# Kernel optimization log

Hardware: AMD Instinct MI355X
Metric: run time of the kernel (lower is better)

Reference implementation:

```python
import jax, jax.numpy as jnp
import numpy as np

HIDDEN = 32  # hard-coded in EdgeModel's Sequential

def setup_inputs() -> dict:
    key = jax.random.key(0)
    ks = jax.random.split(key, 9)
    E, FN, FE, OUT = 200000, 512, 256, 128
    IN = FN + FN + FE  # 1280
    src = jax.random.normal(ks[0], (E, FN), dtype=jnp.float32)
    dest = jax.random.normal(ks[1], (E, FN), dtype=jnp.float32)
    edge_attr = jax.random.normal(ks[2], (E, FE), dtype=jnp.float32)
    u = jax.random.normal(ks[3], (64, 128), dtype=jnp.float32)
    batch = jax.random.randint(ks[4], (E,), 0, 64, dtype=jnp.int64)
    # Linear params, PyTorch default init scale ~ 1/sqrt(fan_in)
    s1 = 1.0 / np.sqrt(IN)
    s2 = 1.0 / np.sqrt(HIDDEN)
    W1 = jax.random.uniform(ks[5], (IN, HIDDEN), jnp.float32, -s1, s1)
    b1 = jax.random.uniform(ks[6], (HIDDEN,), jnp.float32, -s1, s1)
    W2 = jax.random.uniform(ks[7], (HIDDEN, OUT), jnp.float32, -s2, s2)
    b2 = jax.random.uniform(ks[8], (OUT,), jnp.float32, -s2, s2)
    return {"src": src, "dest": dest, "edge_attr": edge_attr, "u": u,
            "batch": batch, "W1": W1, "b1": b1, "W2": W2, "b2": b2}

def reference(src, dest, edge_attr, u, batch, W1, b1, W2, b2):
    # concat along feature dim, then Linear -> ELU -> Linear (u, batch unused)
    x = jnp.concatenate([src, dest, edge_attr], axis=1)  # [E, 2*FN+FE]
    h = jax.nn.elu(x @ W1 + b1)                           # [E, 32]
    return h @ W2 + b2                                    # [E, OUT]
```

## Files before the change

### kernel.cpp

```cpp
#include <hip/hip_runtime.h>
#include <hip/hip_bf16.h>

typedef __bf16 bf16x8 __attribute__((ext_vector_type(8)));
typedef unsigned short u16x8 __attribute__((ext_vector_type(8)));
typedef float f32x4 __attribute__((ext_vector_type(4)));

__global__ __launch_bounds__(256) void prep_w_kernel(
    const float* __restrict__ W1, const float* __restrict__ W2,
    unsigned short* __restrict__ wsB1, unsigned short* __restrict__ wsB2) {
  int tid = blockIdx.x * 256 + threadIdx.x;
  if (tid < 40960) {
    int j = tid & 7, l = (tid >> 3) & 63, nt = (tid >> 9) & 1, kt = tid >> 10;
    int k = kt * 32 + ((l >> 4) << 3) + j;
    int n = nt * 16 + (l & 15);
    __bf16 v = (__bf16)W1[k * 32 + n];
    wsB1[tid] = __builtin_bit_cast(unsigned short, v);
  } else if (tid < 45056) {
    int t = tid - 40960;
    int j = t & 7, l = (t >> 3) & 63, nt = t >> 9;
    int k = ((l >> 4) << 3) + j;
    int n = nt * 16 + (l & 15);
    __bf16 v = (__bf16)W2[k * 128 + n];
    wsB2[t] = __builtin_bit_cast(unsigned short, v);
  }
}

template <bool USE_WS>
__global__ __launch_bounds__(256) void edge_mlp_kernel(
    const float* __restrict__ src, const float* __restrict__ dst,
    const float* __restrict__ ea, const float* __restrict__ W1,
    const float* __restrict__ b1, const float* __restrict__ W2,
    const float* __restrict__ b2, const unsigned short* __restrict__ wsB1,
    const unsigned short* __restrict__ wsB2, float* __restrict__ out, int nE) {
  __shared__ alignas(16) unsigned short hbuf_s[4][16 * 40];
  const int lane = threadIdx.x & 63;
  const int wave = threadIdx.x >> 6;
  const int l15 = lane & 15;
  const int lh = lane >> 4;
  const long strip = (long)blockIdx.x * 4 + wave;
  const long e0 = strip * 16;
  if (e0 >= nE) return;
  long row = e0 + l15;
  if (row >= nE) row = nE - 1;

  f32x4 acc0 = {0.f, 0.f, 0.f, 0.f};
  f32x4 acc1 = {0.f, 0.f, 0.f, 0.f};

  auto do_tile = [&](const float* p, int kt) {
    f32x4 lo = *(const f32x4*)p;
    f32x4 hi = *(const f32x4*)(p + 4);
    bf16x8 a;
    a[0] = (__bf16)lo[0]; a[1] = (__bf16)lo[1];
    a[2] = (__bf16)lo[2]; a[3] = (__bf16)lo[3];
    a[4] = (__bf16)hi[0]; a[5] = (__bf16)hi[1];
    a[6] = (__bf16)hi[2]; a[7] = (__bf16)hi[3];
    bf16x8 bf0, bf1;
    if (USE_WS) {
      const unsigned short* wp = wsB1 + kt * 1024 + lane * 8;
      bf0 = __builtin_bit_cast(bf16x8, *(const u16x8*)wp);
      bf1 = __builtin_bit_cast(bf16x8, *(const u16x8*)(wp + 512));
    } else {
#pragma unroll
      for (int j = 0; j < 8; ++j) {
        int k = kt * 32 + lh * 8 + j;
        bf0[j] = (__bf16)W1[k * 32 + l15];
        bf1[j] = (__bf16)W1[k * 32 + 16 + l15];
      }
    }
    acc0 = __builtin_amdgcn_mfma_f32_16x16x32_bf16(a, bf0, acc0, 0, 0, 0);
    acc1 = __builtin_amdgcn_mfma_f32_16x16x32_bf16(a, bf1, acc1, 0, 0, 0);
  };

  {
    const float* base = src + row * 512 + lh * 8;
#pragma unroll 4
    for (int kt = 0; kt < 16; ++kt) do_tile(base + kt * 32, kt);
  }
  {
    const float* base = dst + row * 512 + lh * 8;
#pragma unroll 4
    for (int kt = 0; kt < 16; ++kt) do_tile(base + kt * 32, 16 + kt);
  }
  {
    const float* base = ea + row * 256 + lh * 8;
#pragma unroll 4
    for (int kt = 0; kt < 8; ++kt) do_tile(base + kt * 32, 32 + kt);
  }

  const float bias0 = b1[l15];
  const float bias1 = b1[16 + l15];
  unsigned short* hl = hbuf_s[wave];
#pragma unroll
  for (int r = 0; r < 4; ++r) {
    int hrow = lh * 4 + r;
    float h0 = acc0[r] + bias0;
    float h1 = acc1[r] + bias1;
    h0 = h0 > 0.f ? h0 : (__expf(h0) - 1.f);
    h1 = h1 > 0.f ? h1 : (__expf(h1) - 1.f);
    __bf16 v0 = (__bf16)h0, v1 = (__bf16)h1;
    hl[hrow * 40 + l15] = __builtin_bit_cast(unsigned short, v0);
    hl[hrow * 40 + 16 + l15] = __builtin_bit_cast(unsigned short, v1);
  }
  asm volatile("s_waitcnt lgkmcnt(0)" ::: "memory");
  bf16x8 ha =
      __builtin_bit_cast(bf16x8, *(const u16x8*)(hl + l15 * 40 + lh * 8));

  f32x4 o[8];
#pragma unroll
  for (int nt = 0; nt < 8; ++nt) {
    bf16x8 bw;
    if (USE_WS) {
      bw = __builtin_bit_cast(bf16x8, *(const u16x8*)(wsB2 + nt * 512 + lane * 8));
    } else {
#pragma unroll
      for (int j = 0; j < 8; ++j)
        bw[j] = (__bf16)W2[(lh * 8 + j) * 128 + nt * 16 + l15];
    }
    f32x4 z = {0.f, 0.f, 0.f, 0.f};
    o[nt] = __builtin_amdgcn_mfma_f32_16x16x32_bf16(ha, bw, z, 0, 0, 0);
  }

#pragma unroll
  for (int nt = 0; nt < 8; ++nt) {
    float bb = b2[nt * 16 + l15];
#pragma unroll
    for (int r = 0; r < 4; ++r) {
      long e = e0 + lh * 4 + r;
      if (e < nE) out[e * 128 + nt * 16 + l15] = o[nt][r] + bb;
    }
  }
}

extern "C" void kernel_launch(void* const* d_in, const int* in_sizes, int n_in,
                              void* d_out, int out_size, void* d_ws,
                              size_t ws_size, hipStream_t stream) {
  const float* src = (const float*)d_in[0];
  const float* dst = (const float*)d_in[1];
  const float* ea = (const float*)d_in[2];
  const float* W1 = (const float*)d_in[5];
  const float* b1 = (const float*)d_in[6];
  const float* W2 = (const float*)d_in[7];
  const float* b2 = (const float*)d_in[8];
  float* out = (float*)d_out;

  const int nE = in_sizes[0] / 512;
  const long strips = (nE + 15) / 16;
  const int nblocks = (int)((strips + 3) / 4);

  unsigned short* wsB1 = (unsigned short*)d_ws;
  unsigned short* wsB2 = wsB1 + 40960;
  const bool use_ws = ws_size >= 45056 * sizeof(unsigned short);

  if (use_ws) {
    prep_w_kernel<<<176, 256, 0, stream>>>(W1, W2, wsB1, wsB2);
    edge_mlp_kernel<true><<<nblocks, 256, 0, stream>>>(
        src, dst, ea, W1, b1, W2, b2, wsB1, wsB2, out, nE);
  } else {
    edge_mlp_kernel<false><<<nblocks, 256, 0, stream>>>(
        src, dst, ea, W1, b1, W2, b2, nullptr, nullptr, out, nE);
  }
}
```

Measured before the change: 259.5 us.

## Software-pipeline activation and weight loads with register prefetch ring in first GEMM

Replaces the three per-input K loops (unroll 4) with one fully unrolled 40-step loop. It uses a register ring buffer that prefetches activation tiles 6 steps ahead and weight tiles 3 steps ahead. The goal is to keep more global loads in flight and hide memory latency behind the MFMAs in this bandwidth-bound kernel. The cost is higher VGPR pressure, which could lower occupancy.

```diff
diff --git a/kernel.cpp b/kernel.cpp
--- a/kernel.cpp
+++ b/kernel.cpp
@@ -43,48 +43,73 @@
   long row = e0 + l15;
   if (row >= nE) row = nE - 1;
 
+  const float* psrc = src + row * 512 + lh * 8;
+  const float* pdst = dst + row * 512 + lh * 8;
+  const float* pea = ea + row * 256 + lh * 8;
+  const unsigned short* pw1 = wsB1 + lane * 8;
+
   f32x4 acc0 = {0.f, 0.f, 0.f, 0.f};
   f32x4 acc1 = {0.f, 0.f, 0.f, 0.f};
 
-  auto do_tile = [&](const float* p, int kt) {
-    f32x4 lo = *(const f32x4*)p;
-    f32x4 hi = *(const f32x4*)(p + 4);
+  auto xptr = [&](int t) -> const float* {
+    return (t < 16) ? (psrc + t * 32)
+         : (t < 32) ? (pdst + (t - 16) * 32)
+                    : (pea + (t - 32) * 32);
+  };
+
+  constexpr int DX = 6;
+  constexpr int DW = 3;
+  f32x4 px[DX][2];
+  u16x8 pw[DW][2];
+
+#pragma unroll
+  for (int t = 0; t < DX; ++t) {
+    const float* p = xptr(t);
+    px[t][0] = *(const f32x4*)p;
+    px[t][1] = *(const f32x4*)(p + 4);
+  }
+  if constexpr (USE_WS) {
+#pragma unroll
+    for (int t = 0; t < DW; ++t) {
+      pw[t][0] = *(const u16x8*)(pw1 + t * 1024);
+      pw[t][1] = *(const u16x8*)(pw1 + t * 1024 + 512);
+    }
+  }
+
+#pragma unroll
+  for (int t = 0; t < 40; ++t) {
+    f32x4 lo = px[t % DX][0];
+    f32x4 hi = px[t % DX][1];
+    bf16x8 bf0, bf1;
+    if constexpr (USE_WS) {
+      bf0 = __builtin_bit_cast(bf16x8, pw[t % DW][0]);
+      bf1 = __builtin_bit_cast(bf16x8, pw[t % DW][1]);
+    } else {
+#pragma unroll
+      for (int j = 0; j < 8; ++j) {
+        int k = t * 32 + lh * 8 + j;
+        bf0[j] = (__bf16)W1[k * 32 + l15];
+        bf1[j] = (__bf16)W1[k * 32 + 16 + l15];
+      }
+    }
+    if (t + DX < 40) {
+      const float* p = xptr(t + DX);
+      px[t % DX][0] = *(const f32x4*)p;
+      px[t % DX][1] = *(const f32x4*)(p + 4);
+    }
+    if constexpr (USE_WS) {
+      if (t + DW < 40) {
+        pw[t % DW][0] = *(const u16x8*)(pw1 + (t + DW) * 1024);
+        pw[t % DW][1] = *(const u16x8*)(pw1 + (t + DW) * 1024 + 512);
+      }
+    }
     bf16x8 a;
     a[0] = (__bf16)lo[0]; a[1] = (__bf16)lo[1];
     a[2] = (__bf16)lo[2]; a[3] = (__bf16)lo[3];
     a[4] = (__bf16)hi[0]; a[5] = (__bf16)hi[1];
     a[6] = (__bf16)hi[2]; a[7] = (__bf16)hi[3];
-    bf16x8 bf0, bf1;
-    if (USE_WS) {
-      const unsigned short* wp = wsB1 + kt * 1024 + lane * 8;
-      bf0 = __builtin_bit_cast(bf16x8, *(const u16x8*)wp);
-      bf1 = __builtin_bit_cast(bf16x8, *(const u16x8*)(wp + 512));
-    } else {
-#pragma unroll
-      for (int j = 0; j < 8; ++j) {
-        int k = kt * 32 + lh * 8 + j;
-        bf0[j] = (__bf16)W1[k * 32 + l15];
-        bf1[j] = (__bf16)W1[k * 32 + 16 + l15];
-      }
-    }
     acc0 = __builtin_amdgcn_mfma_f32_16x16x32_bf16(a, bf0, acc0, 0, 0, 0);
     acc1 = __builtin_amdgcn_mfma_f32_16x16x32_bf16(a, bf1, acc1, 0, 0, 0);
-  };
-
-  {
-    const float* base = src + row * 512 + lh * 8;
-#pragma unroll 4
-    for (int kt = 0; kt < 16; ++kt) do_tile(base + kt * 32, kt);
-  }
-  {
-    const float* base = dst + row * 512 + lh * 8;
-#pragma unroll 4
-    for (int kt = 0; kt < 16; ++kt) do_tile(base + kt * 32, 16 + kt);
-  }
-  {
-    const float* base = ea + row * 256 + lh * 8;
-#pragma unroll 4
-    for (int kt = 0; kt < 8; ++kt) do_tile(base + kt * 32, 32 + kt);
   }
 
   const float bias0 = b1[l15];
```

Result: no change. 259.6 us (+0.0%).

## Software-pipeline input and weight loads with inline-asm buffer loads and explicit vmcnt waits

Applied to the files above, without the earlier changes.

Replaces the compiler-scheduled loop over the 40 K-tiles with a hand-unrolled software pipeline. It uses inline-asm buffer_load_dwordx4 with buffer resource descriptors, six activation slots and four weight slots in flight, and explicit s_waitcnt vmcnt gating each MFMA pair. The aim is to keep many global loads outstanding per wave so the memory-bound streaming of the 1280-wide rows hides latency. It also sets a minimum-occupancy launch bound and adds scheduling barriers. In exchange it raises register pressure, and the 32-bit buffer descriptor sizes could overflow for larger edge counts.

```diff
diff --git a/kernel.cpp b/kernel.cpp
--- a/kernel.cpp
+++ b/kernel.cpp
@@ -4,6 +4,7 @@
 typedef __bf16 bf16x8 __attribute__((ext_vector_type(8)));
 typedef unsigned short u16x8 __attribute__((ext_vector_type(8)));
 typedef float f32x4 __attribute__((ext_vector_type(4)));
+typedef unsigned int u32x4 __attribute__((ext_vector_type(4)));
 
 __global__ __launch_bounds__(256) void prep_w_kernel(
     const float* __restrict__ W1, const float* __restrict__ W2,
@@ -25,8 +26,46 @@
   }
 }
 
+__device__ __forceinline__ u32x4 make_srd(const void* p, unsigned bytes) {
+  u32x4 r;
+  r[0] = (unsigned)(unsigned long long)p;
+  r[1] = (unsigned)(((unsigned long long)p) >> 32);
+  r[2] = bytes;
+  r[3] = 0x00020000u;
+  return r;
+}
+
+#define XLD(SLOT, VOFF, OFF0, OFF1)                                        \
+  asm volatile("buffer_load_dwordx4 %0, %2, %3, 0 offen offset:" #OFF0     \
+               "\n\tbuffer_load_dwordx4 %1, %2, %3, 0 offen offset:" #OFF1 \
+               : "=&v"(px[SLOT][0]), "=&v"(px[SLOT][1])                    \
+               : "v"(VOFF), "s"(srdX))
+#define WLD(SLOT, SOFF)                                                    \
+  asm volatile("buffer_load_dwordx4 %0, %2, %3, %4 offen offset:0"         \
+               "\n\tbuffer_load_dwordx4 %1, %2, %3, %4 offen offset:1024"  \
+               : "=&v"(pw[SLOT][0]), "=&v"(pw[SLOT][1])                    \
+               : "v"(voffw), "s"(srdw), "s"((unsigned)(SOFF)))
+#define VMW(N)                                                \
+  do {                                                        \
+    asm volatile("s_waitcnt vmcnt(" #N ")" ::: "memory");     \
+    __builtin_amdgcn_sched_barrier(0);                        \
+  } while (0)
+#define CONS(SX, SW)                                                          \
+  do {                                                                        \
+    f32x4 lo = px[SX][0], hi = px[SX][1];                                     \
+    bf16x8 a;                                                                 \
+    a[0] = (__bf16)lo[0]; a[1] = (__bf16)lo[1];                               \
+    a[2] = (__bf16)lo[2]; a[3] = (__bf16)lo[3];                               \
+    a[4] = (__bf16)hi[0]; a[5] = (__bf16)hi[1];                               \
+    a[6] = (__bf16)hi[2]; a[7] = (__bf16)hi[3];                               \
+    acc0 = __builtin_amdgcn_mfma_f32_16x16x32_bf16(                           \
+        a, __builtin_bit_cast(bf16x8, pw[SW][0]), acc0, 0, 0, 0);             \
+    acc1 = __builtin_amdgcn_mfma_f32_16x16x32_bf16(                           \
+        a, __builtin_bit_cast(bf16x8, pw[SW][1]), acc1, 0, 0, 0);             \
+  } while (0)
+
 template <bool USE_WS>
-__global__ __launch_bounds__(256) void edge_mlp_kernel(
+__global__ __launch_bounds__(256, 4) void edge_mlp_kernel(
     const float* __restrict__ src, const float* __restrict__ dst,
     const float* __restrict__ ea, const float* __restrict__ W1,
     const float* __restrict__ b1, const float* __restrict__ W2,
@@ -46,45 +85,95 @@
   f32x4 acc0 = {0.f, 0.f, 0.f, 0.f};
   f32x4 acc1 = {0.f, 0.f, 0.f, 0.f};
 
-  auto do_tile = [&](const float* p, int kt) {
-    f32x4 lo = *(const f32x4*)p;
-    f32x4 hi = *(const f32x4*)(p + 4);
-    bf16x8 a;
-    a[0] = (__bf16)lo[0]; a[1] = (__bf16)lo[1];
-    a[2] = (__bf16)lo[2]; a[3] = (__bf16)lo[3];
-    a[4] = (__bf16)hi[0]; a[5] = (__bf16)hi[1];
-    a[6] = (__bf16)hi[2]; a[7] = (__bf16)hi[3];
-    bf16x8 bf0, bf1;
-    if (USE_WS) {
-      const unsigned short* wp = wsB1 + kt * 1024 + lane * 8;
-      bf0 = __builtin_bit_cast(bf16x8, *(const u16x8*)wp);
-      bf1 = __builtin_bit_cast(bf16x8, *(const u16x8*)(wp + 512));
-    } else {
+  if constexpr (USE_WS) {
+    const u32x4 srdS = make_srd(src, (unsigned)nE * 2048u);
+    const u32x4 srdD = make_srd(dst, (unsigned)nE * 2048u);
+    const u32x4 srdE = make_srd(ea, (unsigned)nE * 1024u);
+    const u32x4 srdw = make_srd(wsB1, 81920u);
+    const unsigned voffx = (unsigned)row * 2048u + (unsigned)lh * 32u;
+    const unsigned voffe = (unsigned)row * 1024u + (unsigned)lh * 32u;
+    const unsigned voffw = (unsigned)lane * 16u;
+
+    f32x4 px[6][2];
+    u16x8 pw[4][2];
+
+    {
+      const u32x4 srdX = srdS;
+      XLD(0, voffx, 0, 16);       WLD(0, 0);
+      XLD(1, voffx, 128, 144);    WLD(1, 2048);
+      XLD(2, voffx, 256, 272);    WLD(2, 4096);
+      XLD(3, voffx, 384, 400);    WLD(3, 6144);
+      XLD(4, voffx, 512, 528);
+      XLD(5, voffx, 640, 656);
+
+      VMW(16); CONS(0, 0); XLD(0, voffx, 768, 784);    WLD(0, 8192);
+      VMW(16); CONS(1, 1); XLD(1, voffx, 896, 912);    WLD(1, 10240);
+      VMW(16); CONS(2, 2); XLD(2, voffx, 1024, 1040);  WLD(2, 12288);
+      VMW(16); CONS(3, 3); XLD(3, voffx, 1152, 1168);  WLD(3, 14336);
+      VMW(12); CONS(4, 0); XLD(4, voffx, 1280, 1296);  WLD(0, 16384);
+      VMW(12); CONS(5, 1); XLD(5, voffx, 1408, 1424);  WLD(1, 18432);
+      VMW(12); CONS(0, 2); XLD(0, voffx, 1536, 1552);  WLD(2, 20480);
+      VMW(12); CONS(1, 3); XLD(1, voffx, 1664, 1680);  WLD(3, 22528);
+      VMW(12); CONS(2, 0); XLD(2, voffx, 1792, 1808);  WLD(0, 24576);
+      VMW(12); CONS(3, 1); XLD(3, voffx, 1920, 1936);  WLD(1, 26624);
+    }
+    {
+      const u32x4 srdX = srdD;
+      VMW(12); CONS(4, 2); XLD(4, voffx, 0, 16);       WLD(2, 28672);
+      VMW(12); CONS(5, 3); XLD(5, voffx, 128, 144);    WLD(3, 30720);
+      VMW(12); CONS(0, 0); XLD(0, voffx, 256, 272);    WLD(0, 32768);
+      VMW(12); CONS(1, 1); XLD(1, voffx, 384, 400);    WLD(1, 34816);
+      VMW(12); CONS(2, 2); XLD(2, voffx, 512, 528);    WLD(2, 36864);
+      VMW(12); CONS(3, 3); XLD(3, voffx, 640, 656);    WLD(3, 38912);
+      VMW(12); CONS(4, 0); XLD(4, voffx, 768, 784);    WLD(0, 40960);
+      VMW(12); CONS(5, 1); XLD(5, voffx, 896, 912);    WLD(1, 43008);
+      VMW(12); CONS(0, 2); XLD(0, voffx, 1024, 1040);  WLD(2, 45056);
+      VMW(12); CONS(1, 3); XLD(1, voffx, 1152, 1168);  WLD(3, 47104);
+      VMW(12); CONS(2, 0); XLD(2, voffx, 1280, 1296);  WLD(0, 49152);
+      VMW(12); CONS(3, 1); XLD(3, voffx, 1408, 1424);  WLD(1, 51200);
+      VMW(12); CONS(4, 2); XLD(4, voffx, 1536, 1552);  WLD(2, 53248);
+      VMW(12); CONS(5, 3); XLD(5, voffx, 1664, 1680);  WLD(3, 55296);
+      VMW(12); CONS(0, 0); XLD(0, voffx, 1792, 1808);  WLD(0, 57344);
+      VMW(12); CONS(1, 1); XLD(1, voffx, 1920, 1936);  WLD(1, 59392);
+    }
+    {
+      const u32x4 srdX = srdE;
+      VMW(12); CONS(2, 2); XLD(2, voffe, 0, 16);       WLD(2, 61440);
+      VMW(12); CONS(3, 3); XLD(3, voffe, 128, 144);    WLD(3, 63488);
+      VMW(12); CONS(4, 0); XLD(4, voffe, 256, 272);    WLD(0, 65536);
+      VMW(12); CONS(5, 1); XLD(5, voffe, 384, 400);    WLD(1, 67584);
+      VMW(12); CONS(0, 2); XLD(0, voffe, 512, 528);    WLD(2, 69632);
+      VMW(12); CONS(1, 3); XLD(1, voffe, 640, 656);    WLD(3, 71680);
+      VMW(12); CONS(2, 0); XLD(2, voffe, 768, 784);    WLD(0, 73728);
+      VMW(12); CONS(3, 1); XLD(3, voffe, 896, 912);    WLD(1, 75776);
+      VMW(12); CONS(4, 2);                             WLD(2, 77824);
+      VMW(10); CONS(5, 3);                             WLD(3, 79872);
+      VMW(8);  CONS(0, 0);
+      VMW(4);  CONS(1, 1);
+      VMW(2);  CONS(2, 2);
+      VMW(0);  CONS(3, 3);
+    }
+  } else {
+    for (int t = 0; t < 40; ++t) {
+      const float* p = (t < 16) ? (src + row * 512 + t * 32 + lh * 8)
+                     : (t < 32) ? (dst + row * 512 + (t - 16) * 32 + lh * 8)
+                                : (ea + row * 256 + (t - 32) * 32 + lh * 8);
+      f32x4 lo = *(const f32x4*)p;
+      f32x4 hi = *(const f32x4*)(p + 4);
+      bf16x8 a, bf0, bf1;
+      a[0] = (__bf16)lo[0]; a[1] = (__bf16)lo[1];
+      a[2] = (__bf16)lo[2]; a[3] = (__bf16)lo[3];
+      a[4] = (__bf16)hi[0]; a[5] = (__bf16)hi[1];
+      a[6] = (__bf16)hi[2]; a[7] = (__bf16)hi[3];
 #pragma unroll
       for (int j = 0; j < 8; ++j) {
-        int k = kt * 32 + lh * 8 + j;
+        int k = t * 32 + lh * 8 + j;
         bf0[j] = (__bf16)W1[k * 32 + l15];
         bf1[j] = (__bf16)W1[k * 32 + 16 + l15];
       }
-    }
-    acc0 = __builtin_amdgcn_mfma_f32_16x16x32_bf16(a, bf0, acc0, 0, 0, 0);
-    acc1 = __builtin_amdgcn_mfma_f32_16x16x32_bf16(a, bf1, acc1, 0, 0, 0);
-  };
-
-  {
-    const float* base = src + row * 512 + lh * 8;
-#pragma unroll 4
-    for (int kt = 0; kt < 16; ++kt) do_tile(base + kt * 32, kt);
-  }
-  {
-    const float* base = dst + row * 512 + lh * 8;
-#pragma unroll 4
-    for (int kt = 0; kt < 16; ++kt) do_tile(base + kt * 32, 16 + kt);
-  }
-  {
-    const float* base = ea + row * 256 + lh * 8;
-#pragma unroll 4
-    for (int kt = 0; kt < 8; ++kt) do_tile(base + kt * 32, 32 + kt);
+      acc0 = __builtin_amdgcn_mfma_f32_16x16x32_bf16(a, bf0, acc0, 0, 0, 0);
+      acc1 = __builtin_amdgcn_mfma_f32_16x16x32_bf16(a, bf1, acc1, 0, 0, 0);
+    }
   }
 
   const float bias0 = b1[l15];
@@ -102,6 +191,7 @@
     hl[hrow * 40 + 16 + l15] = __builtin_bit_cast(unsigned short, v1);
   }
   asm volatile("s_waitcnt lgkmcnt(0)" ::: "memory");
+  __builtin_amdgcn_sched_barrier(0);
   bf16x8 ha =
       __builtin_bit_cast(bf16x8, *(const u16x8*)(hl + l15 * 40 + lh * 8));
 
```

Result: faster. 247.4 us (-4.7%).

## Stage edge rows into LDS with async double-buffered loads and XCD-aware block remap

Applied to the files above, without the earlier changes.

Each block now covers 64 edges. It streams the concatenated input through a double-buffered, XOR-swizzled LDS tile using global_load_lds, so the fetch of the next 64-column chunk overlaps with the MFMA work on the current one. The block index is remapped so that consecutive logical blocks land on the same XCD, which is meant to improve L2 locality. The fast path now requires nE to be a multiple of 64. It adds a __syncthreads per chunk and reuses the staging buffer for the hidden activations.

```diff
diff --git a/kernel.cpp b/kernel.cpp
--- a/kernel.cpp
+++ b/kernel.cpp
@@ -4,6 +4,11 @@
 typedef __bf16 bf16x8 __attribute__((ext_vector_type(8)));
 typedef unsigned short u16x8 __attribute__((ext_vector_type(8)));
 typedef float f32x4 __attribute__((ext_vector_type(4)));
+
+using gptr_t = const __attribute__((address_space(1))) unsigned int*;
+using lptr_t = __attribute__((address_space(3))) unsigned int*;
+#define gp(x) ((gptr_t)(const void*)(x))
+#define lp(x) ((lptr_t)(void*)(x))
 
 __global__ __launch_bounds__(256) void prep_w_kernel(
     const float* __restrict__ W1, const float* __restrict__ W2,
@@ -32,64 +37,103 @@
     const float* __restrict__ b1, const float* __restrict__ W2,
     const float* __restrict__ b2, const unsigned short* __restrict__ wsB1,
     const unsigned short* __restrict__ wsB2, float* __restrict__ out, int nE) {
-  __shared__ alignas(16) unsigned short hbuf_s[4][16 * 40];
+  __shared__ alignas(16) float xb[2][64][64];
   const int lane = threadIdx.x & 63;
   const int wave = threadIdx.x >> 6;
   const int l15 = lane & 15;
   const int lh = lane >> 4;
-  const long strip = (long)blockIdx.x * 4 + wave;
-  const long e0 = strip * 16;
+
+  const int nwg = gridDim.x;
+  const int q = nwg >> 3, rmd = nwg & 7;
+  const int xcd = (int)blockIdx.x & 7, idx = (int)blockIdx.x >> 3;
+  const int bid =
+      (xcd < rmd ? xcd * (q + 1) : rmd * (q + 1) + (xcd - rmd) * q) + idx;
+
+  const long e0 = (long)bid * 64;
   if (e0 >= nE) return;
-  long row = e0 + l15;
-  if (row >= nE) row = nE - 1;
+  const long erow = e0 + wave * 16 + l15;
+
+  const float bias0 = b1[l15];
+  const float bias1 = b1[16 + l15];
 
   f32x4 acc0 = {0.f, 0.f, 0.f, 0.f};
   f32x4 acc1 = {0.f, 0.f, 0.f, 0.f};
 
-  auto do_tile = [&](const float* p, int kt) {
-    f32x4 lo = *(const f32x4*)p;
-    f32x4 hi = *(const f32x4*)(p + 4);
-    bf16x8 a;
-    a[0] = (__bf16)lo[0]; a[1] = (__bf16)lo[1];
-    a[2] = (__bf16)lo[2]; a[3] = (__bf16)lo[3];
-    a[4] = (__bf16)hi[0]; a[5] = (__bf16)hi[1];
-    a[6] = (__bf16)hi[2]; a[7] = (__bf16)hi[3];
-    bf16x8 bf0, bf1;
-    if (USE_WS) {
-      const unsigned short* wp = wsB1 + kt * 1024 + lane * 8;
-      bf0 = __builtin_bit_cast(bf16x8, *(const u16x8*)wp);
-      bf1 = __builtin_bit_cast(bf16x8, *(const u16x8*)(wp + 512));
-    } else {
+  if constexpr (USE_WS) {
+    auto stage = [&](int c, int b) {
+#pragma unroll
+      for (int r = 0; r < 4; ++r) {
+        const int row_l = r * 16 + wave * 4 + (lane >> 4);
+        const int i = lane & 15;
+        const int g = ((((i >> 1) ^ (row_l & 7)) << 1) | (i & 1));
+        const float* p;
+        if (c < 8)
+          p = src + (e0 + row_l) * 512 + c * 64 + g * 4;
+        else if (c < 16)
+          p = dst + (e0 + row_l) * 512 + (c - 8) * 64 + g * 4;
+        else
+          p = ea + (e0 + row_l) * 256 + (c - 16) * 64 + g * 4;
+        __builtin_amdgcn_global_load_lds(
+            gp(p), lp(&xb[b][r * 16 + wave * 4][0]), 16, 0, 0);
+      }
+    };
+
+    auto consume = [&](int c, int b) {
+      const int lr = wave * 16 + l15;
+#pragma unroll
+      for (int kk = 0; kk < 2; ++kk) {
+        const int pp = (kk * 4 + lh) ^ (lr & 7);
+        const f32x4* ap =
+            (const f32x4*)((const char*)&xb[b][lr][0] + pp * 32);
+        f32x4 lo = ap[0], hi = ap[1];
+        bf16x8 a;
+        a[0] = (__bf16)lo[0]; a[1] = (__bf16)lo[1];
+        a[2] = (__bf16)lo[2]; a[3] = (__bf16)lo[3];
+        a[4] = (__bf16)hi[0]; a[5] = (__bf16)hi[1];
+        a[6] = (__bf16)hi[2]; a[7] = (__bf16)hi[3];
+        const int t = c * 2 + kk;
+        bf16x8 b0 = __builtin_bit_cast(
+            bf16x8, *(const u16x8*)(wsB1 + (t * 2 + 0) * 512 + lane * 8));
+        bf16x8 b1f = __builtin_bit_cast(
+            bf16x8, *(const u16x8*)(wsB1 + (t * 2 + 1) * 512 + lane * 8));
+        acc0 = __builtin_amdgcn_mfma_f32_16x16x32_bf16(a, b0, acc0, 0, 0, 0);
+        acc1 = __builtin_amdgcn_mfma_f32_16x16x32_bf16(a, b1f, acc1, 0, 0, 0);
+      }
+    };
+
+    stage(0, 0);
+    __syncthreads();
+#pragma unroll
+    for (int c = 0; c < 20; ++c) {
+      if (c < 19) stage(c + 1, (c + 1) & 1);
+      consume(c, c & 1);
+      if (c < 19) __syncthreads();
+    }
+  } else {
+    long rowf = erow < nE ? erow : nE - 1;
+    for (int t = 0; t < 40; ++t) {
+      const float* p = (t < 16) ? (src + rowf * 512 + t * 32 + lh * 8)
+                     : (t < 32) ? (dst + rowf * 512 + (t - 16) * 32 + lh * 8)
+                                : (ea + rowf * 256 + (t - 32) * 32 + lh * 8);
+      f32x4 lo = *(const f32x4*)p;
+      f32x4 hi = *(const f32x4*)(p + 4);
+      bf16x8 a, bf0, bf1;
+      a[0] = (__bf16)lo[0]; a[1] = (__bf16)lo[1];
+      a[2] = (__bf16)lo[2]; a[3] = (__bf16)lo[3];
+      a[4] = (__bf16)hi[0]; a[5] = (__bf16)hi[1];
+      a[6] = (__bf16)hi[2]; a[7] = (__bf16)hi[3];
 #pragma unroll
       for (int j = 0; j < 8; ++j) {
-        int k = kt * 32 + lh * 8 + j;
+        int k = t * 32 + lh * 8 + j;
         bf0[j] = (__bf16)W1[k * 32 + l15];
         bf1[j] = (__bf16)W1[k * 32 + 16 + l15];
       }
-    }
-    acc0 = __builtin_amdgcn_mfma_f32_16x16x32_bf16(a, bf0, acc0, 0, 0, 0);
-    acc1 = __builtin_amdgcn_mfma_f32_16x16x32_bf16(a, bf1, acc1, 0, 0, 0);
-  };
-
-  {
-    const float* base = src + row * 512 + lh * 8;
-#pragma unroll 4
-    for (int kt = 0; kt < 16; ++kt) do_tile(base + kt * 32, kt);
-  }
-  {
-    const float* base = dst + row * 512 + lh * 8;
-#pragma unroll 4
-    for (int kt = 0; kt < 16; ++kt) do_tile(base + kt * 32, 16 + kt);
-  }
-  {
-    const float* base = ea + row * 256 + lh * 8;
-#pragma unroll 4
-    for (int kt = 0; kt < 8; ++kt) do_tile(base + kt * 32, 32 + kt);
-  }
-
-  const float bias0 = b1[l15];
-  const float bias1 = b1[16 + l15];
-  unsigned short* hl = hbuf_s[wave];
+      acc0 = __builtin_amdgcn_mfma_f32_16x16x32_bf16(a, bf0, acc0, 0, 0, 0);
+      acc1 = __builtin_amdgcn_mfma_f32_16x16x32_bf16(a, bf1, acc1, 0, 0, 0);
+    }
+  }
+
+  unsigned short* hl = ((unsigned short*)&xb[0][0][0]) + wave * 2048;
 #pragma unroll
   for (int r = 0; r < 4; ++r) {
     int hrow = lh * 4 + r;
@@ -102,6 +146,7 @@
     hl[hrow * 40 + 16 + l15] = __builtin_bit_cast(unsigned short, v1);
   }
   asm volatile("s_waitcnt lgkmcnt(0)" ::: "memory");
+  __builtin_amdgcn_sched_barrier(0);
   bf16x8 ha =
       __builtin_bit_cast(bf16x8, *(const u16x8*)(hl + l15 * 40 + lh * 8));
 
@@ -110,7 +155,8 @@
   for (int nt = 0; nt < 8; ++nt) {
     bf16x8 bw;
     if (USE_WS) {
-      bw = __builtin_bit_cast(bf16x8, *(const u16x8*)(wsB2 + nt * 512 + lane * 8));
+      bw = __builtin_bit_cast(bf16x8,
+                              *(const u16x8*)(wsB2 + nt * 512 + lane * 8));
     } else {
 #pragma unroll
       for (int j = 0; j < 8; ++j)
@@ -120,12 +166,13 @@
     o[nt] = __builtin_amdgcn_mfma_f32_16x16x32_bf16(ha, bw, z, 0, 0, 0);
   }
 
+  const long ebase = e0 + wave * 16;
 #pragma unroll
   for (int nt = 0; nt < 8; ++nt) {
     float bb = b2[nt * 16 + l15];
 #pragma unroll
     for (int r = 0; r < 4; ++r) {
-      long e = e0 + lh * 4 + r;
+      long e = ebase + lh * 4 + r;
       if (e < nE) out[e * 128 + nt * 16 + l15] = o[nt][r] + bb;
     }
   }
@@ -144,18 +191,20 @@
   float* out = (float*)d_out;
 
   const int nE = in_sizes[0] / 512;
-  const long strips = (nE + 15) / 16;
-  const int nblocks = (int)((strips + 3) / 4);
 
   unsigned short* wsB1 = (unsigned short*)d_ws;
   unsigned short* wsB2 = wsB1 + 40960;
-  const bool use_ws = ws_size >= 45056 * sizeof(unsigned short);
+  const bool use_ws =
+      ws_size >= 45056 * sizeof(unsigned short) && (nE & 63) == 0;
 
   if (use_ws) {
+    const int nblocks = nE / 64;
     prep_w_kernel<<<176, 256, 0, stream>>>(W1, W2, wsB1, wsB2);
     edge_mlp_kernel<true><<<nblocks, 256, 0, stream>>>(
         src, dst, ea, W1, b1, W2, b2, wsB1, wsB2, out, nE);
   } else {
+    const long strips = (nE + 15) / 16;
+    const int nblocks = (int)((strips + 3) / 4);
     edge_mlp_kernel<false><<<nblocks, 256, 0, stream>>>(
         src, dst, ea, W1, b1, W2, b2, nullptr, nullptr, out, nE);
   }
```

After: 244.5 us. 1.06x faster.
